# Kernel tuning notes

Hardware: AMD Instinct MI355X
Metric: run time of the kernel (lower is better)

The kernel has to match this reference:

```python
import jax, jax.numpy as jnp
import numpy as np

# DPConv hyperparameters (from init_kwargs)
KERNEL = 8      # kernel
EXT = 4         # extension
STRIDE = 4      # stride


def _adaptive_bins(K, k):
    # Replicates F.adaptive_avg_pool2d bin boundaries: start=floor(i*K/k), end=ceil((i+1)*K/k)
    i = np.arange(k)
    r0 = np.floor(i * K / k).astype(np.int32)
    r1 = np.ceil((i + 1) * K / k).astype(np.int32)
    return r0, r1


def _dpconv(x):
    N, C, H, W = x.shape
    k, e, s = KERNEL, EXT, STRIDE
    K = k + 2 * e  # unfold window size
    oh = (H - k) // s + 1
    ow = (W - k) // s + 1

    # replicate pad, matching F.pad(..., mode='replicate')
    xp = jnp.pad(x, ((0, 0), (0, 0), (e, e), (e, e)), mode='edge')

    # integral image so each adaptive-pool bin sum is an O(1) 4-point lookup
    # (avoids materializing the (N,C,K,K,num_windows) unfolded tensor)
    I = jnp.cumsum(jnp.cumsum(xp, axis=2), axis=3)
    I = jnp.pad(I, ((0, 0), (0, 0), (1, 0), (1, 0)))  # (N,C,Hp+1,Wp+1)

    r0, r1 = _adaptive_bins(K, k)
    i0 = np.arange(oh) * s  # window top-left rows in padded coords
    j0 = np.arange(ow) * s
    A0 = (i0[:, None] + r0[None, :])  # (oh,k) bin row starts
    A1 = (i0[:, None] + r1[None, :])  # (oh,k) bin row ends
    B0 = (j0[:, None] + r0[None, :])  # (ow,k)
    B1 = (j0[:, None] + r1[None, :])
    area = ((r1 - r0)[:, None] * (r1 - r0)[None, :]).astype(x.dtype)  # (k,k)

    a0 = A0[:, :, None, None]; a1 = A1[:, :, None, None]  # (oh,k,1,1)
    b0 = B0[None, None, :, :]; b1 = B1[None, None, :, :]  # (1,1,ow,k)
    # rectangle sums -> pooled regions (N,C,oh,k,ow,k)
    S = I[:, :, a1, b1] - I[:, :, a0, b1] - I[:, :, a1, b0] + I[:, :, a0, b0]
    pooled = S / area[None, :, None, :]

    # overlap-add fold (kernel k, stride s) + count normalization
    HH = (np.arange(oh) * s)[:, None] + np.arange(k)[None, :]  # (oh,k) output rows
    WW = (np.arange(ow) * s)[:, None] + np.arange(k)[None, :]  # (ow,k) output cols
    hidx = HH[:, :, None, None]
    widx = WW[None, None, :, :]
    out = jnp.zeros((N, C, H, W), dtype=x.dtype).at[:, :, hidx, widx].add(pooled)
    cnt = jnp.zeros((H, W), dtype=x.dtype).at[hidx, widx].add(jnp.ones((oh, k, ow, k), dtype=x.dtype))
    return out / cnt


def setup_inputs() -> dict:
    key = jax.random.key(0)
    x = jax.random.normal(key, (8, 64, 128, 128), dtype=jnp.float32)
    return {"x": x}


def reference(x):
    return _dpconv(x)
```

## Files before the change

kernel.cpp:

```cpp
#include <hip/hip_runtime.h>


#define HH 128
#define WW 128

__global__ __launch_bounds__(256) void dpconv_kernel(const float* __restrict__ x,
                                                     float* __restrict__ out) {
    const int gid = blockIdx.x * 256 + threadIdx.x;
    const int t   = gid & 31;
    const int row = gid >> 5;
    const int h   = row & (HH - 1);

    const float* __restrict__ xp = x + (size_t)(row >> 7) * (HH * WW);
    float* __restrict__ op       = out + (size_t)row * WW;

    const int m  = h & 3;
    const bool v1 = (h < 124);
    const bool v2 = (h >= 4);
    const int ra0 = max(h + m - 4, 0);
    const int ra1 = max(h + m - 3, 0);
    const int rb0 = min(h + m,     127);
    const int rb1 = min(h + m + 1, 127);
    const int c   = t << 2;

    const float4 a0 = *reinterpret_cast<const float4*>(xp + ra0 * WW + c);
    const float4 a1 = *reinterpret_cast<const float4*>(xp + ra1 * WW + c);
    const float4 b0 = *reinterpret_cast<const float4*>(xp + rb0 * WW + c);
    const float4 b1 = *reinterpret_cast<const float4*>(xp + rb1 * WW + c);

    const float g1 = v1 ? 1.0f : 0.0f;
    const float g2 = v2 ? 1.0f : 0.0f;
    const float gs = (v1 && v2) ? 0.25f : 0.5f;

    float4 M;
    M.x = (g1 * (a0.x + a1.x) + g2 * (b0.x + b1.x)) * gs;
    M.y = (g1 * (a0.y + a1.y) + g2 * (b0.y + b1.y)) * gs;
    M.z = (g1 * (a0.z + a1.z) + g2 * (b0.z + b1.z)) * gs;
    M.w = (g1 * (a0.w + a1.w) + g2 * (b0.w + b1.w)) * gs;

    const float s0 = M.x + M.y;
    const float s1 = M.z + M.w;

    float Ls0 = __shfl_up(s0, 1, 32);
    float Ls1 = __shfl_up(s1, 1, 32);
    float Rs0 = __shfl_down(s0, 1, 32);
    float Rs1 = __shfl_down(s1, 1, 32);
    if (t == 0)  { Ls0 = 2.0f * M.x; Ls1 = 2.0f * M.x; }
    if (t == 31) { Rs0 = 2.0f * M.w; Rs1 = 2.0f * M.w; }

    const float f1 = (t < 31) ? 1.0f : 0.0f;
    const float f2 = (t > 0)  ? 1.0f : 0.0f;
    const float sc = (t == 0 || t == 31) ? 0.5f : 0.25f;

    float4 o;
    o.x = (f1 * Ls0 + f2 * s0) * sc;
    o.y = (f1 * Ls1 + f2 * s1) * sc;
    o.z = (f1 * s0 + f2 * Rs0) * sc;
    o.w = (f1 * s1 + f2 * Rs1) * sc;
    *reinterpret_cast<float4*>(op + c) = o;
}

extern "C" void kernel_launch(void* const* d_in, const int* in_sizes, int n_in,
                              void* d_out, int out_size, void* d_ws, size_t ws_size,
                              hipStream_t stream) {
    const float* x = (const float*)d_in[0];
    float* out     = (float*)d_out;
    const int planes  = in_sizes[0] / (HH * WW);
    const int threads = planes * HH * (WW / 4);
    dpconv_kernel<<<threads / 256, 256, 0, stream>>>(x, out);
}
```

Baseline: 85.46 us.

## Stage row tiles in LDS via direct global-to-LDS loads, one block per 32 rows

Each block now loads a 40-row halo tile of one plane into shared memory and computes 32 output rows from it, where before every thread read four rows straight from global memory. When the builtin is available, the tile is fetched with direct global-to-LDS async loads. The aim is to cut redundant global and L2 traffic, since each input row was read about four times. In exchange it adds a barrier, uses 20KB of LDS per block, and launches a quarter as many blocks with four iterations per thread.

```diff
diff --git a/kernel.cpp b/kernel.cpp
--- a/kernel.cpp
+++ b/kernel.cpp
@@ -3,61 +3,97 @@
 
 #define HH 128
 #define WW 128
+#define RCH 32
+#define TROWS (RCH + 8)
 
 __global__ __launch_bounds__(256) void dpconv_kernel(const float* __restrict__ x,
                                                      float* __restrict__ out) {
-    const int gid = blockIdx.x * 256 + threadIdx.x;
-    const int t   = gid & 31;
-    const int row = gid >> 5;
-    const int h   = row & (HH - 1);
+    __shared__ float raw[TROWS][WW];
 
-    const float* __restrict__ xp = x + (size_t)(row >> 7) * (HH * WW);
-    float* __restrict__ op       = out + (size_t)row * WW;
+    const int bid   = blockIdx.x;
+    const int plane = bid >> 2;
+    const int h0    = (bid & 3) * RCH;
 
-    const int m  = h & 3;
-    const bool v1 = (h < 124);
-    const bool v2 = (h >= 4);
-    const int ra0 = max(h + m - 4, 0);
-    const int ra1 = max(h + m - 3, 0);
-    const int rb0 = min(h + m,     127);
-    const int rb1 = min(h + m + 1, 127);
-    const int c   = t << 2;
+    const float* __restrict__ xp = x + (size_t)plane * (HH * WW);
+    float* __restrict__ op       = out + (size_t)plane * (HH * WW) + (size_t)h0 * WW;
 
-    const float4 a0 = *reinterpret_cast<const float4*>(xp + ra0 * WW + c);
-    const float4 a1 = *reinterpret_cast<const float4*>(xp + ra1 * WW + c);
-    const float4 b0 = *reinterpret_cast<const float4*>(xp + rb0 * WW + c);
-    const float4 b1 = *reinterpret_cast<const float4*>(xp + rb1 * WW + c);
+    const int wv = threadIdx.x >> 6;
+    const int ln = threadIdx.x & 63;
+#if __has_builtin(__builtin_amdgcn_global_load_lds)
+    #pragma unroll
+    for (int i = 0; i < 5; ++i) {
+        const int row = wv * 10 + i * 2 + (ln >> 5);
+        const int col = (ln & 31) << 2;
+        const int gr  = min(max(h0 - 4 + row, 0), HH - 1);
+        const float* src = xp + gr * WW + col;
+        __builtin_amdgcn_global_load_lds(
+            (__attribute__((address_space(1))) void*)src,
+            (__attribute__((address_space(3))) void*)((char*)&raw[0][0] + wv * 5120 + i * 1024),
+            16, 0, 0);
+    }
+#else
+    for (int idx = threadIdx.x; idx < TROWS * 32; idx += 256) {
+        const int row = idx >> 5;
+        const int col = (idx & 31) << 2;
+        const int gr  = min(max(h0 - 4 + row, 0), HH - 1);
+        *reinterpret_cast<float4*>(&raw[row][col]) =
+            *reinterpret_cast<const float4*>(xp + gr * WW + col);
+    }
+#endif
+    __syncthreads();
 
-    const float g1 = v1 ? 1.0f : 0.0f;
-    const float g2 = v2 ? 1.0f : 0.0f;
-    const float gs = (v1 && v2) ? 0.25f : 0.5f;
+    #pragma unroll
+    for (int it = 0; it < 4; ++it) {
+        const int e  = it * 256 + (int)threadIdx.x;
+        const int hr = e >> 5;
+        const int t  = e & 31;
+        const int h  = h0 + hr;
+        const int m  = h & 3;
+        const bool v1 = (h < 124);
+        const bool v2 = (h >= 4);
+        const int lbase = 4 - h0;
+        const int la0 = max(h + m - 4, 0) + lbase;
+        const int la1 = max(h + m - 3, 0) + lbase;
+        const int lb0 = min(h + m,     127) + lbase;
+        const int lb1 = min(h + m + 1, 127) + lbase;
+        const int c   = t << 2;
 
-    float4 M;
-    M.x = (g1 * (a0.x + a1.x) + g2 * (b0.x + b1.x)) * gs;
-    M.y = (g1 * (a0.y + a1.y) + g2 * (b0.y + b1.y)) * gs;
-    M.z = (g1 * (a0.z + a1.z) + g2 * (b0.z + b1.z)) * gs;
-    M.w = (g1 * (a0.w + a1.w) + g2 * (b0.w + b1.w)) * gs;
+        const float4 a0 = *reinterpret_cast<const float4*>(&raw[la0][c]);
+        const float4 a1 = *reinterpret_cast<const float4*>(&raw[la1][c]);
+        const float4 b0 = *reinterpret_cast<const float4*>(&raw[lb0][c]);
+        const float4 b1 = *reinterpret_cast<const float4*>(&raw[lb1][c]);
 
-    const float s0 = M.x + M.y;
-    const float s1 = M.z + M.w;
+        const float g1 = v1 ? 1.0f : 0.0f;
+        const float g2 = v2 ? 1.0f : 0.0f;
+        const float gs = (v1 && v2) ? 0.25f : 0.5f;
 
-    float Ls0 = __shfl_up(s0, 1, 32);
-    float Ls1 = __shfl_up(s1, 1, 32);
-    float Rs0 = __shfl_down(s0, 1, 32);
-    float Rs1 = __shfl_down(s1, 1, 32);
-    if (t == 0)  { Ls0 = 2.0f * M.x; Ls1 = 2.0f * M.x; }
-    if (t == 31) { Rs0 = 2.0f * M.w; Rs1 = 2.0f * M.w; }
+        float4 M;
+        M.x = (g1 * (a0.x + a1.x) + g2 * (b0.x + b1.x)) * gs;
+        M.y = (g1 * (a0.y + a1.y) + g2 * (b0.y + b1.y)) * gs;
+        M.z = (g1 * (a0.z + a1.z) + g2 * (b0.z + b1.z)) * gs;
+        M.w = (g1 * (a0.w + a1.w) + g2 * (b0.w + b1.w)) * gs;
 
-    const float f1 = (t < 31) ? 1.0f : 0.0f;
-    const float f2 = (t > 0)  ? 1.0f : 0.0f;
-    const float sc = (t == 0 || t == 31) ? 0.5f : 0.25f;
+        const float s0 = M.x + M.y;
+        const float s1 = M.z + M.w;
 
-    float4 o;
-    o.x = (f1 * Ls0 + f2 * s0) * sc;
-    o.y = (f1 * Ls1 + f2 * s1) * sc;
-    o.z = (f1 * s0 + f2 * Rs0) * sc;
-    o.w = (f1 * s1 + f2 * Rs1) * sc;
-    *reinterpret_cast<float4*>(op + c) = o;
+        float Ls0 = __shfl_up(s0, 1, 32);
+        float Ls1 = __shfl_up(s1, 1, 32);
+        float Rs0 = __shfl_down(s0, 1, 32);
+        float Rs1 = __shfl_down(s1, 1, 32);
+        if (t == 0)  { Ls0 = 2.0f * M.x; Ls1 = 2.0f * M.x; }
+        if (t == 31) { Rs0 = 2.0f * M.w; Rs1 = 2.0f * M.w; }
+
+        const float f1 = (t < 31) ? 1.0f : 0.0f;
+        const float f2 = (t > 0)  ? 1.0f : 0.0f;
+        const float sc = (t == 0 || t == 31) ? 0.5f : 0.25f;
+
+        float4 o;
+        o.x = (f1 * Ls0 + f2 * s0) * sc;
+        o.y = (f1 * Ls1 + f2 * s1) * sc;
+        o.z = (f1 * s0 + f2 * Rs0) * sc;
+        o.w = (f1 * s1 + f2 * Rs1) * sc;
+        *reinterpret_cast<float4*>(op + hr * WW + c) = o;
+    }
 }
 
 extern "C" void kernel_launch(void* const* d_in, const int* in_sizes, int n_in,
@@ -65,7 +101,6 @@
                               hipStream_t stream) {
     const float* x = (const float*)d_in[0];
     float* out     = (float*)d_out;
-    const int planes  = in_sizes[0] / (HH * WW);
-    const int threads = planes * HH * (WW / 4);
-    dpconv_kernel<<<threads / 256, 256, 0, stream>>>(x, out);
+    const int planes = in_sizes[0] / (HH * WW);
+    dpconv_kernel<<<planes * (HH / RCH), 256, 0, stream>>>(x, out);
 }
```

After: 80.20 us. 6.2% less time.
